# Kernel tuning notes

Hardware: AMD Instinct MI355X
Metric: run time of the kernel (lower is better)

The kernel has to match this reference:

```python
import jax, jax.numpy as jnp
import numpy as np

N = 100000          # nodes
E = 1600000         # edges (avg degree 16)
D_IN = 128
D_OUT = 128
K = 3               # Chebyshev order
LAMBDA_MAX = 2.0    # PyG default for sym normalization


def setup_inputs() -> dict:
    key = jax.random.key(0)
    k1, k2, k3, k4 = jax.random.split(key, 4)
    x = jax.random.normal(k1, (N, D_IN), dtype=jnp.float32)
    edge_index = jax.random.randint(k2, (2, E), 0, N, dtype=jnp.int32)
    # Glorot-ish init for the K per-order linear weights
    weight = jax.random.normal(k3, (K, D_IN, D_OUT), dtype=jnp.float32) * (1.0 / np.sqrt(D_IN))
    bias = jax.random.normal(k4, (D_OUT,), dtype=jnp.float32) * 0.01
    return {"x": x, "edge_index": edge_index, "weight": weight, "bias": bias}


def reference(x, edge_index, weight, bias):
    src, dst = edge_index[0], edge_index[1]
    n = x.shape[0]

    # remove self loops (zero their weight), symmetric normalization
    ew = jnp.where(src != dst, 1.0, 0.0).astype(x.dtype)
    deg = jax.ops.segment_sum(ew, src, num_segments=n)
    dis = jnp.where(deg > 0, jax.lax.rsqrt(jnp.maximum(deg, 1.0)), 0.0)
    norm = dis[src] * ew * dis[dst]          # D^-1/2 A D^-1/2 entries

    # scaled Laplacian T-hat = (2/lmax) L - I, L = I - A_norm
    off_w = -(2.0 / LAMBDA_MAX) * norm       # off-diagonal entries
    diag_w = 2.0 / LAMBDA_MAX - 1.0          # = 0 for lambda_max=2

    def spmm(h):  # T-hat @ h : gather-multiply-scatter over edges
        agg = jax.ops.segment_sum(off_w[:, None] * h[src], dst, num_segments=n)
        return agg + diag_w * h

    # Chebyshev recurrence: Tx_k = 2 T-hat Tx_{k-1} - Tx_{k-2}
    Tx0 = x
    out = Tx0 @ weight[0]
    Tx1 = spmm(Tx0)
    out = out + Tx1 @ weight[1]
    for k in range(2, weight.shape[0]):
        Tx2 = 2.0 * spmm(Tx1) - Tx0
        out = out + Tx2 @ weight[k]
        Tx0, Tx1 = Tx1, Tx2
    return out + bias
```

## Files before the change

kernel.cpp:

```cpp
#include <hip/hip_runtime.h>
#include <hip/hip_bf16.h>

typedef __hip_bfloat16 bf16;
typedef __attribute__((ext_vector_type(8))) short short8;
typedef __attribute__((ext_vector_type(4))) float float4v;

#define N_NODES 100000
#define M_PAD   100096
#define N_EDGES 1600000
#define D 128
#define K_CAT 384
#define BUCKET_CAP 56
#define NBIN 392
#define BIN_CAP 4608
#define CHUNK 4096

__device__ __forceinline__ float b2f(bf16 v) { return __bfloat162float(v); }
__device__ __forceinline__ bf16 f2b(float v) { return __float2bfloat16(v); }
__device__ __forceinline__ float us2f(unsigned short u) {
    unsigned int x = ((unsigned int)u) << 16;
    return __uint_as_float(x);
}
__device__ __forceinline__ float ub(unsigned int u, int k) {
    return (float)((u >> (k * 8)) & 0xffu);
}

__global__ void prep_w_kernel(const float* __restrict__ w, const float* __restrict__ bias,
                              bf16* __restrict__ wT, float* __restrict__ biasf) {
    int i = blockIdx.x * blockDim.x + threadIdx.x;
    if (i < D * K_CAT) {
        int o = i / K_CAT, k = i % K_CAT;
        float v;
        if (k < 128) {
            v = w[k * D + o] - w[2 * 16384 + k * D + o];
        } else if (k < 256) {
            v = w[16384 + (k - 128) * D + o];
        } else {
            v = 2.0f * w[2 * 16384 + (k - 256) * D + o];
        }
        wT[i] = f2b(v);
    }
    if (i < D) biasf[i] = bias[i];
}

__global__ __launch_bounds__(256) void quantx_kernel(const float* __restrict__ x,
                                                     const float* __restrict__ dis,
                                                     unsigned char* __restrict__ xq,
                                                     float* __restrict__ dsx0) {
    int wv = threadIdx.x >> 6, lane = threadIdx.x & 63;
    int n = blockIdx.x * 4 + wv;
    float2 v = *(const float2*)(x + (size_t)n * D + lane * 2);
    float m = fmaxf(fabsf(v.x), fabsf(v.y));
#pragma unroll
    for (int k = 1; k < 64; k <<= 1) m = fmaxf(m, __shfl_xor(m, k));
    float inv = (m > 0.0f) ? 127.0f / m : 0.0f;
    int q0 = (int)rintf(v.x * inv) + 128;
    int q1 = (int)rintf(v.y * inv) + 128;
    *(unsigned short*)(xq + (size_t)n * D + lane * 2) =
        (unsigned short)((q0 & 0xff) | ((q1 & 0xff) << 8));
    if (lane == 0) dsx0[n] = dis[n] * (m * (1.0f / 127.0f));
}

__global__ __launch_bounds__(256) void phaseA_kernel(const int* __restrict__ src,
                                                     const int* __restrict__ dst,
                                                     int* __restrict__ gCursD,
                                                     int* __restrict__ gCursS,
                                                     unsigned int* __restrict__ gBinD,
                                                     unsigned char* __restrict__ gBinS) {
    __shared__ int histD[NBIN], histS[NBIN], cursD[NBIN], cursS[NBIN];
    int tid = threadIdx.x;
    for (int t = tid; t < NBIN; t += 256) { histD[t] = 0; histS[t] = 0; }
    __syncthreads();
    int e0 = blockIdx.x * CHUNK;
    for (int i = tid; i < CHUNK; i += 256) {
        int e = e0 + i;
        if (e >= N_EDGES) break;
        int s = src[e], d = dst[e];
        if (s == d) continue;
        atomicAdd(&histD[d >> 8], 1);
        atomicAdd(&histS[s >> 8], 1);
    }
    __syncthreads();
    for (int t = tid; t < NBIN; t += 256) {
        cursD[t] = (histD[t] > 0) ? atomicAdd(&gCursD[t], histD[t]) : 0;
        cursS[t] = (histS[t] > 0) ? atomicAdd(&gCursS[t], histS[t]) : 0;
    }
    __syncthreads();
    for (int i = tid; i < CHUNK; i += 256) {
        int e = e0 + i;
        if (e >= N_EDGES) break;
        int s = src[e], d = dst[e];
        if (s == d) continue;
        int bd = d >> 8, bs = s >> 8;
        int sd = atomicAdd(&cursD[bd], 1);
        if (sd < BIN_CAP) gBinD[(size_t)bd * BIN_CAP + sd] = ((unsigned int)s << 8) | (unsigned int)(d & 255);
        int ss = atomicAdd(&cursS[bs], 1);
        if (ss < BIN_CAP) gBinS[(size_t)bs * BIN_CAP + ss] = (unsigned char)(s & 255);
    }
}

__global__ __launch_bounds__(256) void phaseB_kernel(const int* __restrict__ gCursD,
                                                     const int* __restrict__ gCursS,
                                                     const unsigned int* __restrict__ gBinD,
                                                     const unsigned char* __restrict__ gBinS,
                                                     int* __restrict__ cnt,
                                                     float* __restrict__ dis,
                                                     int* __restrict__ bucket) {
    __shared__ int curs[256];
    int tid = threadIdx.x;
    int b = blockIdx.x;
    curs[tid] = 0;
    __syncthreads();
    if (b < NBIN) {
        int count = min(gCursD[b], BIN_CAP);
        const unsigned int* rec = gBinD + (size_t)b * BIN_CAP;
        int n0 = b << 8;
        for (int j = tid; j < count; j += 256) {
            unsigned int r = rec[j];
            int dloc = r & 255;
            int s = (int)(r >> 8);
            int slot = atomicAdd(&curs[dloc], 1);
            if (slot < BUCKET_CAP) bucket[(size_t)(n0 + dloc) * BUCKET_CAP + slot] = s;
        }
        __syncthreads();
        int n = n0 + tid;
        if (n < N_NODES) cnt[n] = curs[tid];
    } else {
        int bb = b - NBIN;
        int count = min(gCursS[bb], BIN_CAP);
        const unsigned char* rec = gBinS + (size_t)bb * BIN_CAP;
        for (int j = tid; j < count; j += 256) {
            atomicAdd(&curs[rec[j]], 1);
        }
        __syncthreads();
        int n = (bb << 8) + tid;
        if (n < N_NODES) {
            int c = curs[tid];
            dis[n] = (c > 0) ? rsqrtf((float)c) : 0.0f;
        }
    }
}

template<int OUTQ>
__global__ __launch_bounds__(256) void spmm_q_kernel(const unsigned char* __restrict__ hq,
                                                     const float* __restrict__ dsx,
                                                     const float* __restrict__ dis,
                                                     const int* __restrict__ cnt,
                                                     const int* __restrict__ bucket,
                                                     unsigned char* __restrict__ outq,
                                                     float* __restrict__ oscale,
                                                     float* __restrict__ odsx,
                                                     bf16* __restrict__ outb) {
    int wv = threadIdx.x >> 6;
    int lane = threadIdx.x & 63;
    int n = blockIdx.x * 4 + wv;
    int c = min(cnt[n], BUCKET_CAP);
    float dn = dis[n];
    int q = lane >> 4;
    int r = lane & 15;
    int s_l = 0;
    float w_l = 0.0f;
    if (lane < c) {
        s_l = bucket[(size_t)n * BUCKET_CAP + lane];
        w_l = -dsx[s_l] * dn;
    }
    float acc[8];
#pragma unroll
    for (int k = 0; k < 8; k++) acc[k] = 0.0f;
    float cw = 0.0f;
    for (int j0 = 0; j0 < c; j0 += 8) {
        int jA = j0 + q;
        int jB = j0 + 4 + q;
        int sA = __shfl(s_l, jA);
        int sB = __shfl(s_l, jB);
        float wA = __shfl(w_l, jA);
        float wB = __shfl(w_l, jB);
        uint2 uA = *(const uint2*)(hq + (size_t)sA * D + (r << 3));
        uint2 uB = *(const uint2*)(hq + (size_t)sB * D + (r << 3));
        cw += wA + wB;
        acc[0] += wA * ub(uA.x, 0) + wB * ub(uB.x, 0);
        acc[1] += wA * ub(uA.x, 1) + wB * ub(uB.x, 1);
        acc[2] += wA * ub(uA.x, 2) + wB * ub(uB.x, 2);
        acc[3] += wA * ub(uA.x, 3) + wB * ub(uB.x, 3);
        acc[4] += wA * ub(uA.y, 0) + wB * ub(uB.y, 0);
        acc[5] += wA * ub(uA.y, 1) + wB * ub(uB.y, 1);
        acc[6] += wA * ub(uA.y, 2) + wB * ub(uB.y, 2);
        acc[7] += wA * ub(uA.y, 3) + wB * ub(uB.y, 3);
    }
#pragma unroll
    for (int k = 0; k < 8; k++) {
        acc[k] += __shfl_xor(acc[k], 16);
        acc[k] += __shfl_xor(acc[k], 32);
    }
    cw += __shfl_xor(cw, 16);
    cw += __shfl_xor(cw, 32);
#pragma unroll
    for (int k = 0; k < 8; k++) acc[k] -= 128.0f * cw;

    if (OUTQ) {
        float m = 0.0f;
#pragma unroll
        for (int k = 0; k < 8; k++) m = fmaxf(m, fabsf(acc[k]));
#pragma unroll
        for (int k = 1; k < 16; k <<= 1) m = fmaxf(m, __shfl_xor(m, k));
        float inv = (m > 0.0f) ? 127.0f / m : 0.0f;
        if (q == 0) {
            unsigned int b0 = 0, b1 = 0;
#pragma unroll
            for (int k = 0; k < 4; k++)
                b0 |= ((unsigned int)((int)rintf(acc[k] * inv) + 128) & 0xffu) << (8 * k);
#pragma unroll
            for (int k = 0; k < 4; k++)
                b1 |= ((unsigned int)((int)rintf(acc[4 + k] * inv) + 128) & 0xffu) << (8 * k);
            uint2 pk; pk.x = b0; pk.y = b1;
            *(uint2*)(outq + (size_t)n * D + (r << 3)) = pk;
            if (lane == 0) {
                float sc = m * (1.0f / 127.0f);
                oscale[n] = sc;
                odsx[n] = dn * sc;
            }
        }
    } else {
        if (q == 0) {
            unsigned int p0 = (unsigned int)__bfloat16_as_ushort(f2b(acc[0])) |
                              ((unsigned int)__bfloat16_as_ushort(f2b(acc[1])) << 16);
            unsigned int p1 = (unsigned int)__bfloat16_as_ushort(f2b(acc[2])) |
                              ((unsigned int)__bfloat16_as_ushort(f2b(acc[3])) << 16);
            unsigned int p2 = (unsigned int)__bfloat16_as_ushort(f2b(acc[4])) |
                              ((unsigned int)__bfloat16_as_ushort(f2b(acc[5])) << 16);
            unsigned int p3 = (unsigned int)__bfloat16_as_ushort(f2b(acc[6])) |
                              ((unsigned int)__bfloat16_as_ushort(f2b(acc[7])) << 16);
            uint4 pk; pk.x = p0; pk.y = p1; pk.z = p2; pk.w = p3;
            *(uint4*)(outb + (size_t)n * D + (r << 3)) = pk;
        }
    }
}

#define AS_STRIDE 40
__global__ __launch_bounds__(256) void gemm_kernel(const float* __restrict__ x,
                                                   const unsigned char* __restrict__ tx1q,
                                                   const float* __restrict__ tx1scale,
                                                   const bf16* __restrict__ agg2,
                                                   const bf16* __restrict__ wT,
                                                   const float* __restrict__ biasf,
                                                   float* __restrict__ out) {
    __shared__ bf16 As[128 * AS_STRIDE];
    __shared__ bf16 Bs[128 * AS_STRIDE];

    int tid = threadIdx.x;
    int nb = blockIdx.x * 128;
    int w = tid >> 6;
    int lane = tid & 63;
    int lq = lane >> 4;
    int lr = lane & 15;

    float4v acc[2][8];
#pragma unroll
    for (int i = 0; i < 2; i++)
#pragma unroll
        for (int j = 0; j < 8; j++) acc[i][j] = (float4v)0.0f;

    for (int kc = 0; kc < 12; kc++) {
        int kbase = kc * 32;
        if (kc < 4) {
#pragma unroll
            for (int t = 0; t < 4; t++) {
                int c = tid + t * 256;
                int row = c >> 3;
                int off = (c & 7) * 4;
                int gr = nb + row;
                if (gr > N_NODES - 1) gr = N_NODES - 1;
                float4 v = *(const float4*)(x + (size_t)gr * D + kbase + off);
                unsigned int p0 = (unsigned int)__bfloat16_as_ushort(f2b(v.x)) |
                                  ((unsigned int)__bfloat16_as_ushort(f2b(v.y)) << 16);
                unsigned int p1 = (unsigned int)__bfloat16_as_ushort(f2b(v.z)) |
                                  ((unsigned int)__bfloat16_as_ushort(f2b(v.w)) << 16);
                uint2 pk; pk.x = p0; pk.y = p1;
                *(uint2*)(As + row * AS_STRIDE + off) = pk;
            }
        } else if (kc < 8) {
            int soff = (kc & 3) * 32;
#pragma unroll
            for (int t = 0; t < 2; t++) {
                int c = tid + t * 256;
                int row = c >> 2;
                int off = (c & 3) * 8;
                int gr = nb + row;
                uint2 u = *(const uint2*)(tx1q + (size_t)gr * D + soff + off);
                float sc = tx1scale[gr];
                float f0 = sc * (ub(u.x, 0) - 128.0f);
                float f1 = sc * (ub(u.x, 1) - 128.0f);
                float f2 = sc * (ub(u.x, 2) - 128.0f);
                float f3 = sc * (ub(u.x, 3) - 128.0f);
                float f4 = sc * (ub(u.y, 0) - 128.0f);
                float f5 = sc * (ub(u.y, 1) - 128.0f);
                float f6 = sc * (ub(u.y, 2) - 128.0f);
                float f7 = sc * (ub(u.y, 3) - 128.0f);
                uint4 pk;
                pk.x = (unsigned int)__bfloat16_as_ushort(f2b(f0)) |
                       ((unsigned int)__bfloat16_as_ushort(f2b(f1)) << 16);
                pk.y = (unsigned int)__bfloat16_as_ushort(f2b(f2)) |
                       ((unsigned int)__bfloat16_as_ushort(f2b(f3)) << 16);
                pk.z = (unsigned int)__bfloat16_as_ushort(f2b(f4)) |
                       ((unsigned int)__bfloat16_as_ushort(f2b(f5)) << 16);
                pk.w = (unsigned int)__bfloat16_as_ushort(f2b(f6)) |
                       ((unsigned int)__bfloat16_as_ushort(f2b(f7)) << 16);
                *(uint4*)(As + row * AS_STRIDE + off) = pk;
            }
        } else {
            int soff = (kc & 3) * 32;
#pragma unroll
            for (int t = 0; t < 2; t++) {
                int c = tid + t * 256;
                int row = c >> 2;
                int off = (c & 3) * 8;
                uint4 v = *(const uint4*)(agg2 + (size_t)(nb + row) * D + soff + off);
                *(uint4*)(As + row * AS_STRIDE + off) = v;
            }
        }
#pragma unroll
        for (int t = 0; t < 2; t++) {
            int c = tid + t * 256;
            int row = c >> 2;
            int off = (c & 3) * 8;
            uint4 v = *(const uint4*)(wT + (size_t)row * K_CAT + kbase + off);
            *(uint4*)(Bs + row * AS_STRIDE + off) = v;
        }
        __syncthreads();

        short8 af[2], bfr[8];
#pragma unroll
        for (int i = 0; i < 2; i++)
            af[i] = *(const short8*)(As + (w * 32 + i * 16 + lr) * AS_STRIDE + lq * 8);
#pragma unroll
        for (int j = 0; j < 8; j++)
            bfr[j] = *(const short8*)(Bs + (j * 16 + lr) * AS_STRIDE + lq * 8);
#pragma unroll
        for (int i = 0; i < 2; i++)
#pragma unroll
            for (int j = 0; j < 8; j++)
                acc[i][j] = __builtin_amdgcn_mfma_f32_16x16x32_bf16(af[i], bfr[j], acc[i][j], 0, 0, 0);
        __syncthreads();
    }

#pragma unroll
    for (int i = 0; i < 2; i++) {
        int rowb = nb + w * 32 + i * 16 + lq * 4;
#pragma unroll
        for (int j = 0; j < 8; j++) {
            int col = j * 16 + lr;
            float bv = biasf[col];
#pragma unroll
            for (int r = 0; r < 4; r++) {
                int row = rowb + r;
                if (row < N_NODES) out[(size_t)row * D + col] = acc[i][j][r] + bv;
            }
        }
    }
}

extern "C" void kernel_launch(void* const* d_in, const int* in_sizes, int n_in,
                              void* d_out, int out_size, void* d_ws, size_t ws_size,
                              hipStream_t stream) {
    const float* x    = (const float*)d_in[0];
    const int*   ei   = (const int*)d_in[1];
    const float* w    = (const float*)d_in[2];
    const float* bias = (const float*)d_in[3];
    float* out = (float*)d_out;

    char* p = (char*)d_ws;
    int*   cnt      = (int*)p;     p += (size_t)N_NODES * 4;
    float* dis      = (float*)p;   p += (size_t)N_NODES * 4;
    int*   gCurs    = (int*)p;     p += (size_t)2 * NBIN * 4;
    float* dsx0     = (float*)p;   p += (size_t)M_PAD * 4;
    float* tx1scale = (float*)p;   p += (size_t)M_PAD * 4;
    float* dsx1     = (float*)p;   p += (size_t)M_PAD * 4;
    int*   bucket   = (int*)p;     p += (size_t)N_NODES * BUCKET_CAP * 4;
    char*  buf1     = p;           p += (size_t)M_PAD * D * 2;
    bf16*  buf2     = (bf16*)p;    p += (size_t)M_PAD * D * 2;
    bf16*  wT       = (bf16*)p;    p += (size_t)D * K_CAT * 2;
    float* biasf    = (float*)p;   p += (size_t)D * 4;

    int*   gCursD = gCurs;
    int*   gCursS = gCurs + NBIN;
    unsigned int*  gBinD = (unsigned int*)buf1;
    unsigned char* gBinS = (unsigned char*)(gBinD + (size_t)NBIN * BIN_CAP);
    unsigned char* xq   = (unsigned char*)buf1;
    unsigned char* tx1q = xq + (size_t)M_PAD * D;
    bf16* agg2 = buf2;

    hipMemsetAsync(gCurs, 0, (size_t)2 * NBIN * 4, stream);

    prep_w_kernel<<<(D * K_CAT + 255) / 256, 256, 0, stream>>>(w, bias, wT, biasf);
    phaseA_kernel<<<(N_EDGES + CHUNK - 1) / CHUNK, 256, 0, stream>>>(ei, ei + N_EDGES,
                                                                     gCursD, gCursS, gBinD, gBinS);
    phaseB_kernel<<<2 * NBIN, 256, 0, stream>>>(gCursD, gCursS, gBinD, gBinS, cnt, dis, bucket);
    quantx_kernel<<<N_NODES / 4, 256, 0, stream>>>(x, dis, xq, dsx0);
    spmm_q_kernel<1><<<N_NODES / 4, 256, 0, stream>>>(xq, dsx0, dis, cnt, bucket,
                                                      tx1q, tx1scale, dsx1, (bf16*)nullptr);
    spmm_q_kernel<0><<<N_NODES / 4, 256, 0, stream>>>(tx1q, dsx1, dis, cnt, bucket,
                                                      (unsigned char*)nullptr, (float*)nullptr,
                                                      (float*)nullptr, agg2);
    gemm_kernel<<<M_PAD / 128, 256, 0, stream>>>(x, tx1q, tx1scale, agg2, wT, biasf, out);
}
```

Measured before the change: 324.2 us.

## Software-pipeline SpMM gathers with packed byte conversion and split edge binning by side

The SpMM inner loop now prefetches the next pair of quantized neighbor rows before it accumulates the current pair, so gather latency is hidden behind arithmetic. Accumulation uses float2 vectors fed by v_cvt_f32_ubyte inline asm, which enables packed FMA and removes the shift-and-mask byte extraction. The edge-binning kernel is split so each block handles either the dst side or the src side, with half-sized chunks and twice as many blocks. This gives more parallelism and smaller shared-memory histograms, at the cost of reading the edge list twice. Prefetching past the last valid neighbor reads row 0 with zero weight, which adds a small amount of redundant traffic.

Result: slower. 333.7 us (+2.9%).

```diff
diff --git a/kernel.cpp b/kernel.cpp
--- a/kernel.cpp
+++ b/kernel.cpp
@@ -4,6 +4,7 @@
 typedef __hip_bfloat16 bf16;
 typedef __attribute__((ext_vector_type(8))) short short8;
 typedef __attribute__((ext_vector_type(4))) float float4v;
+typedef __attribute__((ext_vector_type(2))) float float2v;
 
 #define N_NODES 100000
 #define M_PAD   100096
@@ -13,16 +14,27 @@
 #define BUCKET_CAP 56
 #define NBIN 392
 #define BIN_CAP 4608
-#define CHUNK 4096
+#define CHUNK 2048
+#define NCHUNKA 782
 
 __device__ __forceinline__ float b2f(bf16 v) { return __bfloat162float(v); }
 __device__ __forceinline__ bf16 f2b(float v) { return __float2bfloat16(v); }
-__device__ __forceinline__ float us2f(unsigned short u) {
-    unsigned int x = ((unsigned int)u) << 16;
-    return __uint_as_float(x);
-}
 __device__ __forceinline__ float ub(unsigned int u, int k) {
     return (float)((u >> (k * 8)) & 0xffu);
+}
+__device__ __forceinline__ float2v cvt2lo(unsigned int u) {
+    float a, b;
+    asm("v_cvt_f32_ubyte0 %0, %2\n\t"
+        "v_cvt_f32_ubyte1 %1, %2"
+        : "=&v"(a), "=&v"(b) : "v"(u));
+    float2v o; o.x = a; o.y = b; return o;
+}
+__device__ __forceinline__ float2v cvt2hi(unsigned int u) {
+    float a, b;
+    asm("v_cvt_f32_ubyte2 %0, %2\n\t"
+        "v_cvt_f32_ubyte3 %1, %2"
+        : "=&v"(a), "=&v"(b) : "v"(u));
+    float2v o; o.x = a; o.y = b; return o;
 }
 
 __global__ void prep_w_kernel(const float* __restrict__ w, const float* __restrict__ bias,
@@ -67,35 +79,39 @@
                                                      int* __restrict__ gCursS,
                                                      unsigned int* __restrict__ gBinD,
                                                      unsigned char* __restrict__ gBinS) {
-    __shared__ int histD[NBIN], histS[NBIN], cursD[NBIN], cursS[NBIN];
+    __shared__ int hist[NBIN], curs[NBIN];
     int tid = threadIdx.x;
-    for (int t = tid; t < NBIN; t += 256) { histD[t] = 0; histS[t] = 0; }
-    __syncthreads();
-    int e0 = blockIdx.x * CHUNK;
-    for (int i = tid; i < CHUNK; i += 256) {
-        int e = e0 + i;
-        if (e >= N_EDGES) break;
-        int s = src[e], d = dst[e];
-        if (s == d) continue;
-        atomicAdd(&histD[d >> 8], 1);
-        atomicAdd(&histS[s >> 8], 1);
-    }
-    __syncthreads();
-    for (int t = tid; t < NBIN; t += 256) {
-        cursD[t] = (histD[t] > 0) ? atomicAdd(&gCursD[t], histD[t]) : 0;
-        cursS[t] = (histS[t] > 0) ? atomicAdd(&gCursS[t], histS[t]) : 0;
-    }
+    int b = blockIdx.x;
+    int sideS = (b >= NCHUNKA);
+    int e0 = (sideS ? b - NCHUNKA : b) * CHUNK;
+    for (int t = tid; t < NBIN; t += 256) hist[t] = 0;
     __syncthreads();
     for (int i = tid; i < CHUNK; i += 256) {
         int e = e0 + i;
         if (e >= N_EDGES) break;
         int s = src[e], d = dst[e];
         if (s == d) continue;
-        int bd = d >> 8, bs = s >> 8;
-        int sd = atomicAdd(&cursD[bd], 1);
-        if (sd < BIN_CAP) gBinD[(size_t)bd * BIN_CAP + sd] = ((unsigned int)s << 8) | (unsigned int)(d & 255);
-        int ss = atomicAdd(&cursS[bs], 1);
-        if (ss < BIN_CAP) gBinS[(size_t)bs * BIN_CAP + ss] = (unsigned char)(s & 255);
+        atomicAdd(&hist[(sideS ? s : d) >> 8], 1);
+    }
+    __syncthreads();
+    int* gC = sideS ? gCursS : gCursD;
+    for (int t = tid; t < NBIN; t += 256)
+        curs[t] = (hist[t] > 0) ? atomicAdd(&gC[t], hist[t]) : 0;
+    __syncthreads();
+    for (int i = tid; i < CHUNK; i += 256) {
+        int e = e0 + i;
+        if (e >= N_EDGES) break;
+        int s = src[e], d = dst[e];
+        if (s == d) continue;
+        if (!sideS) {
+            int bd = d >> 8;
+            int sd = atomicAdd(&curs[bd], 1);
+            if (sd < BIN_CAP) gBinD[(size_t)bd * BIN_CAP + sd] = ((unsigned int)s << 8) | (unsigned int)(d & 255);
+        } else {
+            int bs = s >> 8;
+            int ss = atomicAdd(&curs[bs], 1);
+            if (ss < BIN_CAP) gBinS[(size_t)bs * BIN_CAP + ss] = (unsigned char)(s & 255);
+        }
     }
 }
 
@@ -164,29 +180,43 @@
         s_l = bucket[(size_t)n * BUCKET_CAP + lane];
         w_l = -dsx[s_l] * dn;
     }
+    const unsigned char* hr = hq + (r << 3);
+
+    float2v acc2[4];
+#pragma unroll
+    for (int k = 0; k < 4; k++) acc2[k] = (float2v)0.0f;
+    float cw = 0.0f;
+
+    int sA = __shfl(s_l, q), sB = __shfl(s_l, 4 + q);
+    float wA = __shfl(w_l, q), wB = __shfl(w_l, 4 + q);
+    uint2 uA = *(const uint2*)(hr + (size_t)sA * D);
+    uint2 uB = *(const uint2*)(hr + (size_t)sB * D);
+
+    for (int j0 = 0; j0 < c; j0 += 8) {
+        int nj = j0 + 8;
+        int sA2 = __shfl(s_l, nj + q);
+        int sB2 = __shfl(s_l, nj + 4 + q);
+        float wA2 = __shfl(w_l, nj + q);
+        float wB2 = __shfl(w_l, nj + 4 + q);
+        uint2 uA2 = *(const uint2*)(hr + (size_t)sA2 * D);
+        uint2 uB2 = *(const uint2*)(hr + (size_t)sB2 * D);
+        cw += wA + wB;
+        float2v wAv; wAv.x = wA; wAv.y = wA;
+        float2v wBv; wBv.x = wB; wBv.y = wB;
+        acc2[0] += wAv * cvt2lo(uA.x);
+        acc2[1] += wAv * cvt2hi(uA.x);
+        acc2[2] += wAv * cvt2lo(uA.y);
+        acc2[3] += wAv * cvt2hi(uA.y);
+        acc2[0] += wBv * cvt2lo(uB.x);
+        acc2[1] += wBv * cvt2hi(uB.x);
+        acc2[2] += wBv * cvt2lo(uB.y);
+        acc2[3] += wBv * cvt2hi(uB.y);
+        sA = sA2; sB = sB2; wA = wA2; wB = wB2; uA = uA2; uB = uB2;
+    }
+
     float acc[8];
 #pragma unroll
-    for (int k = 0; k < 8; k++) acc[k] = 0.0f;
-    float cw = 0.0f;
-    for (int j0 = 0; j0 < c; j0 += 8) {
-        int jA = j0 + q;
-        int jB = j0 + 4 + q;
-        int sA = __shfl(s_l, jA);
-        int sB = __shfl(s_l, jB);
-        float wA = __shfl(w_l, jA);
-        float wB = __shfl(w_l, jB);
-        uint2 uA = *(const uint2*)(hq + (size_t)sA * D + (r << 3));
-        uint2 uB = *(const uint2*)(hq + (size_t)sB * D + (r << 3));
-        cw += wA + wB;
-        acc[0] += wA * ub(uA.x, 0) + wB * ub(uB.x, 0);
-        acc[1] += wA * ub(uA.x, 1) + wB * ub(uB.x, 1);
-        acc[2] += wA * ub(uA.x, 2) + wB * ub(uB.x, 2);
-        acc[3] += wA * ub(uA.x, 3) + wB * ub(uB.x, 3);
-        acc[4] += wA * ub(uA.y, 0) + wB * ub(uB.y, 0);
-        acc[5] += wA * ub(uA.y, 1) + wB * ub(uB.y, 1);
-        acc[6] += wA * ub(uA.y, 2) + wB * ub(uB.y, 2);
-        acc[7] += wA * ub(uA.y, 3) + wB * ub(uB.y, 3);
-    }
+    for (int k = 0; k < 4; k++) { acc[2 * k] = acc2[k].x; acc[2 * k + 1] = acc2[k].y; }
 #pragma unroll
     for (int k = 0; k < 8; k++) {
         acc[k] += __shfl_xor(acc[k], 16);
@@ -392,8 +422,8 @@
     hipMemsetAsync(gCurs, 0, (size_t)2 * NBIN * 4, stream);
 
     prep_w_kernel<<<(D * K_CAT + 255) / 256, 256, 0, stream>>>(w, bias, wT, biasf);
-    phaseA_kernel<<<(N_EDGES + CHUNK - 1) / CHUNK, 256, 0, stream>>>(ei, ei + N_EDGES,
-                                                                     gCursD, gCursS, gBinD, gBinS);
+    phaseA_kernel<<<2 * NCHUNKA, 256, 0, stream>>>(ei, ei + N_EDGES,
+                                                   gCursD, gCursS, gBinD, gBinS);
     phaseB_kernel<<<2 * NBIN, 256, 0, stream>>>(gCursD, gCursS, gBinD, gBinS, cnt, dis, bucket);
     quantx_kernel<<<N_NODES / 4, 256, 0, stream>>>(x, dis, xq, dsx0);
     spmm_q_kernel<1><<<N_NODES / 4, 256, 0, stream>>>(xq, dsx0, dis, cnt, bucket,
```
